# Kernel tuning notes

Measured on AMD Instinct MI355X. Metric: run time of the kernel, lower is better.

The kernel has to match this reference:

```python
import jax, jax.numpy as jnp
import numpy as np

B, I, O, ORDER = 16384, 256, 256, 8
LO, HI = -1.0, 1.0


def setup_inputs() -> dict:
    key = jax.random.key(0)
    k1, k2, k3 = jax.random.split(key, 3)
    x = jax.random.normal(k1, (B, I), dtype=jnp.float32)
    weights = jax.random.normal(k2, (O, I), dtype=jnp.float32)
    # BernsteinBasisFunction init: randn(order+1) * 0.1, one per (o, i) pair
    coeffs = jax.random.normal(k3, (O, I, ORDER + 1), dtype=jnp.float32) * 0.1
    return {"x": x, "weights": weights, "coeffs": coeffs}


def reference(x, weights, coeffs):
    # x: [B, I]; weights: [O, I]; coeffs: [O, I, K+1]
    K = coeffs.shape[-1] - 1
    zoom = (HI - LO) / 2.0
    pan = (HI + LO) / 2.0
    xt = jnp.tanh(x) * zoom + pan          # squash into [LO, HI]
    x_a = xt - LO                          # [B, I]
    x_b = HI - xt                          # [B, I]
    e = jnp.arange(K + 1)
    # ber[b, i, k] = x_a^k * x_b^(K-k)  (unnormalized Bernstein basis)
    ber = (x_a[..., None] ** e) * (x_b[..., None] ** (K - e))  # [B, I, K+1]
    # transformed[b, o, i] = sum_k coeffs[o,i,k] * ber[b,i,k]; out = einsum('boi,oi->bo')
    # Fused: fold weights into coeffs to avoid the [B, O, I] intermediate.
    wc = coeffs * weights[..., None]       # [O, I, K+1]
    return jnp.einsum('bik,oik->bo', ber, wc)
```

## Files before the change

### kernel.cpp

```cpp
#include <hip/hip_runtime.h>
#include <hip/hip_bf16.h>


#define BDIM 16384
#define IDIM 256
#define ODIM 256
#define NK 9
#define ICHUNK 64
#define NCHUNK (IDIM / ICHUNK)
#define NSTEP (NCHUNK * NK)
#define STEP_ELEMS (ODIM * ICHUNK)

typedef short short8 __attribute__((ext_vector_type(8)));
typedef float floatx4 __attribute__((ext_vector_type(4)));

__global__ __launch_bounds__(256) void prep_wc2(const float* __restrict__ weights,
                                                const float* __restrict__ coeffs,
                                                ushort* __restrict__ wc) {
    int idx  = blockIdx.x * 256 + threadIdx.x;
    int step = idx >> 11;
    int c    = idx & 2047;
    int big    = c >> 6;
    int lane_w = c & 63;
    int o    = (big >> 1) * 16 + (lane_w & 15);
    int s    = big & 1;
    int quad = lane_w >> 4;
    int ic = step / 9;
    int k  = step - ic * 9;
    int i0 = ic * 64 + s * 32 + quad * 8;

    const float* cp = coeffs + (size_t)(o * IDIM + i0) * NK + k;
    float4 w0 = *(const float4*)(weights + o * IDIM + i0);
    float4 w1 = *(const float4*)(weights + o * IDIM + i0 + 4);
    float wv[8] = {w0.x, w0.y, w0.z, w0.w, w1.x, w1.y, w1.z, w1.w};

    union { ushort us[8]; int4 v; __hip_bfloat162 h2[4]; } pk;
#pragma unroll
    for (int j = 0; j < 8; j += 2) {
        float a = cp[(size_t)j * NK] * wv[j];
        float b = cp[(size_t)(j + 1) * NK] * wv[j + 1];
        pk.h2[j >> 1] = __float22bfloat162_rn(make_float2(a, b));
    }
    *(int4*)(wc + (size_t)step * STEP_ELEMS + (size_t)c * 8) = pk.v;
}

__global__ __launch_bounds__(256) void bern_gemm(const float* __restrict__ x,
                                                 const ushort* __restrict__ wc,
                                                 float* __restrict__ out) {
    __shared__ ushort A_lds[2][4096];

    const int tid  = threadIdx.x;
    const int wave = tid >> 6;
    const int lane = tid & 63;
    const int row0 = blockIdx.x * 64;

    const int ra0 = tid >> 3;
    const int jg  = tid & 7;
    const int rows_a[2] = { ra0, 32 + ra0 };
    int aoff[2];
#pragma unroll
    for (int u = 0; u < 2; ++u) {
        int rr = rows_a[u];
        aoff[u] = ((((jg >> 2) * 4 + (rr >> 4)) * 64) + (rr & 15) + (jg & 3) * 16) * 8;
    }

    floatx4 acc[4][4];
    floatx4 zero = {0.0f, 0.0f, 0.0f, 0.0f};
#pragma unroll
    for (int m = 0; m < 4; ++m)
#pragma unroll
        for (int n = 0; n < 4; ++n)
            acc[m][n] = zero;

    float p_[2][8], r_[2][8];
    float4 xa0[2], xa1[2];

#pragma unroll
    for (int u = 0; u < 2; ++u) {
        const float* xp = x + (size_t)(row0 + rows_a[u]) * IDIM + jg * 8;
        xa0[u] = *(const float4*)(xp);
        xa1[u] = *(const float4*)(xp + 4);
    }

    for (int ic = 0; ic < NCHUNK; ++ic) {
#pragma unroll
        for (int u = 0; u < 2; ++u) {
            float xv[8] = {xa0[u].x, xa0[u].y, xa0[u].z, xa0[u].w,
                           xa1[u].x, xa1[u].y, xa1[u].z, xa1[u].w};
#pragma unroll
            for (int e = 0; e < 8; ++e) {
                float t = __builtin_amdgcn_exp2f(xv[e] * 2.8853900817779268f);
                float q = 2.0f * __builtin_amdgcn_rcpf(t + 1.0f);
                float q2 = q * q;
                float q4 = q2 * q2;
                p_[u][e] = q4 * q4;
                r_[u][e] = t;
            }
        }
        if (ic < NCHUNK - 1) {
#pragma unroll
            for (int u = 0; u < 2; ++u) {
                const float* xp = x + (size_t)(row0 + rows_a[u]) * IDIM + (ic + 1) * ICHUNK + jg * 8;
                xa0[u] = *(const float4*)(xp);
                xa1[u] = *(const float4*)(xp + 4);
            }
        }

#pragma unroll
        for (int k = 0; k < NK; ++k) {
            const int step = ic * NK + k;
            const int buf  = step & 1;

            short8 bfr[2][4];
            const ushort* wstep = wc + (size_t)step * STEP_ELEMS;
#pragma unroll
            for (int s = 0; s < 2; ++s)
#pragma unroll
                for (int n = 0; n < 4; ++n) {
                    int nglob = wave * 4 + n;
                    bfr[s][n] = *(const short8*)(wstep + ((nglob * 2 + s) * 64 + lane) * 8);
                }

#pragma unroll
            for (int u = 0; u < 2; ++u) {
                union { ushort us[8]; int4 v; __hip_bfloat162 h2[4]; } pk;
#pragma unroll
                for (int e = 0; e < 8; e += 2) {
                    pk.h2[e >> 1] = __float22bfloat162_rn(make_float2(p_[u][e], p_[u][e + 1]));
                    p_[u][e]     *= r_[u][e];
                    p_[u][e + 1] *= r_[u][e + 1];
                }
                *(int4*)&A_lds[buf][aoff[u]] = pk.v;
            }

            __syncthreads();

#pragma unroll
            for (int s = 0; s < 2; ++s) {
                short8 af[4];
#pragma unroll
                for (int m = 0; m < 4; ++m)
                    af[m] = *(const short8*)&A_lds[buf][((s * 4 + m) * 64 + lane) * 8];
#pragma unroll
                for (int m = 0; m < 4; ++m)
#pragma unroll
                    for (int n = 0; n < 4; ++n)
                        acc[m][n] = __builtin_amdgcn_mfma_f32_16x16x32_bf16(
                            af[m], bfr[s][n], acc[m][n], 0, 0, 0);
            }
        }
    }

#pragma unroll
    for (int m = 0; m < 4; ++m) {
#pragma unroll
        for (int n = 0; n < 4; ++n) {
            int col   = wave * 64 + n * 16 + (lane & 15);
            int rbase = row0 + m * 16 + (lane >> 4) * 4;
#pragma unroll
            for (int reg = 0; reg < 4; ++reg) {
                out[(size_t)(rbase + reg) * ODIM + col] = acc[m][n][reg];
            }
        }
    }
}

extern "C" void kernel_launch(void* const* d_in, const int* in_sizes, int n_in,
                              void* d_out, int out_size, void* d_ws, size_t ws_size,
                              hipStream_t stream) {
    const float* x       = (const float*)d_in[0];
    const float* weights = (const float*)d_in[1];
    const float* coeffs  = (const float*)d_in[2];
    float* out = (float*)d_out;
    ushort* wc = (ushort*)d_ws;

    prep_wc2<<<(NSTEP * STEP_ELEMS / 8) / 256, 256, 0, stream>>>(weights, coeffs, wc);
    bern_gemm<<<BDIM / 64, 256, 0, stream>>>(x, wc, out);
}
```

Measured before the change: 98.22 us.

## Build Bernstein A-fragments in registers, drop LDS and barriers, prefetch B fragments

Each wave now computes the Bernstein basis values for its own MFMA A-fragment layout directly in registers. This removes the shared-memory staging and the per-step __syncthreads. The block tile shrinks from 64 to 32 rows, which doubles the grid and sets launch bounds to 2 blocks per SM. The weight fragments are double-buffered in registers so the global loads for the next step overlap the current MFMAs. In exchange, every wave redundantly computes tanh/exp for all 32 rows and reads B from global twice as often overall, because each block covers fewer rows.

```diff
diff --git a/kernel.cpp b/kernel.cpp
--- a/kernel.cpp
+++ b/kernel.cpp
@@ -6,10 +6,9 @@
 #define IDIM 256
 #define ODIM 256
 #define NK 9
-#define ICHUNK 64
-#define NCHUNK (IDIM / ICHUNK)
-#define NSTEP (NCHUNK * NK)
-#define STEP_ELEMS (ODIM * ICHUNK)
+#define NCHUNK 4
+#define NSTEP 36
+#define STEP_ELEMS (ODIM * 64)
 
 typedef short short8 __attribute__((ext_vector_type(8)));
 typedef float floatx4 __attribute__((ext_vector_type(4)));
@@ -44,115 +43,121 @@
     *(int4*)(wc + (size_t)step * STEP_ELEMS + (size_t)c * 8) = pk.v;
 }
 
-__global__ __launch_bounds__(256) void bern_gemm(const float* __restrict__ x,
-                                                 const ushort* __restrict__ wc,
-                                                 float* __restrict__ out) {
-    __shared__ ushort A_lds[2][4096];
-
+__global__ __launch_bounds__(256, 2) void bern_gemm(const float* __restrict__ x,
+                                                    const ushort* __restrict__ wc,
+                                                    float* __restrict__ out) {
     const int tid  = threadIdx.x;
     const int wave = tid >> 6;
     const int lane = tid & 63;
-    const int row0 = blockIdx.x * 64;
+    const int row0 = blockIdx.x * 32;
+    const int lrow = lane & 15;
+    const int jseg = (lane >> 4) * 8;
 
-    const int ra0 = tid >> 3;
-    const int jg  = tid & 7;
-    const int rows_a[2] = { ra0, 32 + ra0 };
-    int aoff[2];
-#pragma unroll
-    for (int u = 0; u < 2; ++u) {
-        int rr = rows_a[u];
-        aoff[u] = ((((jg >> 2) * 4 + (rr >> 4)) * 64) + (rr & 15) + (jg & 3) * 16) * 8;
-    }
-
-    floatx4 acc[4][4];
+    float p[2][2][8];
+    float r[2][2][8];
+    float xc[2][2][8];
+    floatx4 acc[2][4];
     floatx4 zero = {0.0f, 0.0f, 0.0f, 0.0f};
 #pragma unroll
-    for (int m = 0; m < 4; ++m)
+    for (int m = 0; m < 2; ++m)
 #pragma unroll
         for (int n = 0; n < 4; ++n)
             acc[m][n] = zero;
 
-    float p_[2][8], r_[2][8];
-    float4 xa0[2], xa1[2];
+#define LOAD_XCHUNK(ic_)                                                        \
+    {                                                                           \
+        _Pragma("unroll") for (int m = 0; m < 2; ++m)                           \
+        _Pragma("unroll") for (int s = 0; s < 2; ++s) {                         \
+            const float* xp = x + (size_t)(row0 + m * 16 + lrow) * IDIM         \
+                              + (ic_) * 64 + s * 32 + jseg;                     \
+            float4 v0 = *(const float4*)(xp);                                   \
+            float4 v1 = *(const float4*)(xp + 4);                               \
+            xc[m][s][0] = v0.x; xc[m][s][1] = v0.y;                             \
+            xc[m][s][2] = v0.z; xc[m][s][3] = v0.w;                             \
+            xc[m][s][4] = v1.x; xc[m][s][5] = v1.y;                             \
+            xc[m][s][6] = v1.z; xc[m][s][7] = v1.w;                             \
+        }                                                                       \
+    }
+
+#define SETUP_BASIS()                                                           \
+    {                                                                           \
+        _Pragma("unroll") for (int m = 0; m < 2; ++m)                           \
+        _Pragma("unroll") for (int s = 0; s < 2; ++s)                           \
+        _Pragma("unroll") for (int e = 0; e < 8; ++e) {                         \
+            float t  = __builtin_amdgcn_exp2f(xc[m][s][e] * 2.8853900817779268f);\
+            float q  = 2.0f * __builtin_amdgcn_rcpf(t + 1.0f);                  \
+            float q2 = q * q;                                                   \
+            float q4 = q2 * q2;                                                 \
+            p[m][s][e] = q4 * q4;                                               \
+            r[m][s][e] = t;                                                     \
+        }                                                                       \
+    }
+
+    LOAD_XCHUNK(0);
+    SETUP_BASIS();
+    LOAD_XCHUNK(1);
+
+    short8 bfr[2][2][4];
+    {
+        const ushort* w0p = wc;
+#pragma unroll
+        for (int s = 0; s < 2; ++s)
+#pragma unroll
+            for (int n = 0; n < 4; ++n)
+                bfr[0][s][n] = *(const short8*)(w0p + (((wave * 4 + n) * 2 + s) * 64 + lane) * 8);
+    }
 
 #pragma unroll
-    for (int u = 0; u < 2; ++u) {
-        const float* xp = x + (size_t)(row0 + rows_a[u]) * IDIM + jg * 8;
-        xa0[u] = *(const float4*)(xp);
-        xa1[u] = *(const float4*)(xp + 4);
-    }
-
     for (int ic = 0; ic < NCHUNK; ++ic) {
-#pragma unroll
-        for (int u = 0; u < 2; ++u) {
-            float xv[8] = {xa0[u].x, xa0[u].y, xa0[u].z, xa0[u].w,
-                           xa1[u].x, xa1[u].y, xa1[u].z, xa1[u].w};
-#pragma unroll
-            for (int e = 0; e < 8; ++e) {
-                float t = __builtin_amdgcn_exp2f(xv[e] * 2.8853900817779268f);
-                float q = 2.0f * __builtin_amdgcn_rcpf(t + 1.0f);
-                float q2 = q * q;
-                float q4 = q2 * q2;
-                p_[u][e] = q4 * q4;
-                r_[u][e] = t;
-            }
-        }
-        if (ic < NCHUNK - 1) {
-#pragma unroll
-            for (int u = 0; u < 2; ++u) {
-                const float* xp = x + (size_t)(row0 + rows_a[u]) * IDIM + (ic + 1) * ICHUNK + jg * 8;
-                xa0[u] = *(const float4*)(xp);
-                xa1[u] = *(const float4*)(xp + 4);
-            }
-        }
-
 #pragma unroll
         for (int k = 0; k < NK; ++k) {
             const int step = ic * NK + k;
-            const int buf  = step & 1;
+            const int cur  = step & 1;
+            const int nxt  = cur ^ 1;
 
-            short8 bfr[2][4];
-            const ushort* wstep = wc + (size_t)step * STEP_ELEMS;
+            if (step + 1 < NSTEP) {
+                const ushort* wnp = wc + (size_t)(step + 1) * STEP_ELEMS;
+#pragma unroll
+                for (int s = 0; s < 2; ++s)
+#pragma unroll
+                    for (int n = 0; n < 4; ++n)
+                        bfr[nxt][s][n] = *(const short8*)(wnp + (((wave * 4 + n) * 2 + s) * 64 + lane) * 8);
+            }
+
+            short8 af[2][2];
+#pragma unroll
+            for (int m = 0; m < 2; ++m)
+#pragma unroll
+                for (int s = 0; s < 2; ++s) {
+                    union { ushort us[8]; short8 v; __hip_bfloat162 h2[4]; } pk;
+#pragma unroll
+                    for (int e = 0; e < 8; e += 2) {
+                        pk.h2[e >> 1] = __float22bfloat162_rn(
+                            make_float2(p[m][s][e], p[m][s][e + 1]));
+                        p[m][s][e]     *= r[m][s][e];
+                        p[m][s][e + 1] *= r[m][s][e + 1];
+                    }
+                    af[m][s] = pk.v;
+                }
+
 #pragma unroll
             for (int s = 0; s < 2; ++s)
 #pragma unroll
-                for (int n = 0; n < 4; ++n) {
-                    int nglob = wave * 4 + n;
-                    bfr[s][n] = *(const short8*)(wstep + ((nglob * 2 + s) * 64 + lane) * 8);
-                }
-
-#pragma unroll
-            for (int u = 0; u < 2; ++u) {
-                union { ushort us[8]; int4 v; __hip_bfloat162 h2[4]; } pk;
-#pragma unroll
-                for (int e = 0; e < 8; e += 2) {
-                    pk.h2[e >> 1] = __float22bfloat162_rn(make_float2(p_[u][e], p_[u][e + 1]));
-                    p_[u][e]     *= r_[u][e];
-                    p_[u][e + 1] *= r_[u][e + 1];
-                }
-                *(int4*)&A_lds[buf][aoff[u]] = pk.v;
-            }
-
-            __syncthreads();
-
-#pragma unroll
-            for (int s = 0; s < 2; ++s) {
-                short8 af[4];
-#pragma unroll
-                for (int m = 0; m < 4; ++m)
-                    af[m] = *(const short8*)&A_lds[buf][((s * 4 + m) * 64 + lane) * 8];
-#pragma unroll
-                for (int m = 0; m < 4; ++m)
+                for (int m = 0; m < 2; ++m)
 #pragma unroll
                     for (int n = 0; n < 4; ++n)
                         acc[m][n] = __builtin_amdgcn_mfma_f32_16x16x32_bf16(
-                            af[m], bfr[s][n], acc[m][n], 0, 0, 0);
-            }
+                            af[m][s], bfr[cur][s][n], acc[m][n], 0, 0, 0);
+        }
+
+        if (ic < NCHUNK - 1) {
+            SETUP_BASIS();
+            if (ic < NCHUNK - 2) LOAD_XCHUNK(ic + 2);
         }
     }
 
 #pragma unroll
-    for (int m = 0; m < 4; ++m) {
+    for (int m = 0; m < 2; ++m) {
 #pragma unroll
         for (int n = 0; n < 4; ++n) {
             int col   = wave * 64 + n * 16 + (lane & 15);
@@ -163,6 +168,8 @@
             }
         }
     }
+#undef LOAD_XCHUNK
+#undef SETUP_BASIS
 }
 
 extern "C" void kernel_launch(void* const* d_in, const int* in_sizes, int n_in,
@@ -174,6 +181,6 @@
     float* out = (float*)d_out;
     ushort* wc = (ushort*)d_ws;
 
-    prep_wc2<<<(NSTEP * STEP_ELEMS / 8) / 256, 256, 0, stream>>>(weights, coeffs, wc);
-    bern_gemm<<<BDIM / 64, 256, 0, stream>>>(x, wc, out);
+    prep_wc2<<<288, 256, 0, stream>>>(weights, coeffs, wc);
+    bern_gemm<<<BDIM / 32, 256, 0, stream>>>(x, wc, out);
 }
```

Result: slower. 106.1 us (+8.0%).
